# Optimization experiments

Hardware: AMD Instinct MI355X
Metric: run time of the kernel (lower is better)

## Reference

```python
import jax, jax.numpy as jnp
import numpy as np

_LOG2PI = 0.9189385332046727
_NUM_VARS = 256   # D
_NUM_UNITS = 64   # K
_BATCH = 2048     # B
_NUM_LEVELS = 8   # log2(D)


def setup_inputs() -> dict:
    key = jax.random.key(0)
    D, K, B = _NUM_VARS, _NUM_UNITS, _BATCH
    inp = {}
    inp["x"] = jax.random.normal(jax.random.fold_in(key, 0), (B, 1, D), dtype=jnp.float32)
    inp["mu"] = jax.random.normal(jax.random.fold_in(key, 1), (D, K), dtype=jnp.float32)
    inp["log_sigma"] = 0.1 * jax.random.normal(jax.random.fold_in(key, 2), (D, K), dtype=jnp.float32)
    # input-layer bookkeeping: each fold reads one (permuted) variable of x
    inp["in_scope_idx"] = jax.random.permutation(jax.random.fold_in(key, 3), D)[:, None]
    F = D
    for l in range(1, _NUM_LEVELS + 1):
        # fold bookkeeping: irregular pairing of previous-layer folds (permutation -> valid partition)
        inp[f"fold_idx{l}"] = jax.random.permutation(jax.random.fold_in(key, 10 + l), F).reshape(F // 2, 2)
        F //= 2
        inp[f"w{l}"] = jax.random.normal(jax.random.fold_in(key, 100 + l), (F, K, K), dtype=jnp.float32)
    return inp


def _circuit(x, mu, log_sigma, ws, in_scope_idx, fold_idxs):
    # input layer gather: x (B,C,D) -> x[..., idx] (B,C,F,s) -> permute (F,C,B,s)
    xg = jnp.transpose(x[..., in_scope_idx], (2, 1, 0, 3))  # (D,1,B,1)
    xv = xg[:, 0, :, 0]  # (D,B): C=1, scope size 1
    # Gaussian input layer, log densities: (F=D, B, K)
    z = (xv[:, :, None] - mu[:, None, :]) * jnp.exp(-log_sigma)[:, None, :]
    out = -0.5 * z * z - log_sigma[:, None, :] - _LOG2PI
    for fidx, w in zip(fold_idxs, ws):
        # folded Hadamard product layer: gather (F,2,B,K) via bookkeeping, add in log-space
        h = out[fidx].sum(axis=1)  # (F,B,K)
        # folded dense sum layer: y[f,b,j] = logsumexp_k( log softmax(w)[f,j,k] + h[f,b,k] )
        wp = jax.nn.softmax(w, axis=-1)  # (F,K,K)
        m = jnp.max(h, axis=-1, keepdims=True)
        out = jnp.log(jnp.einsum('fbk,fjk->fbj', jnp.exp(h - m), wp)) + m  # (F,B,K)
    # final bookkeeping: (F_out=1, B, K) -> transpose(0,1) -> (B, 1, K)
    return jnp.transpose(out, (1, 0, 2))


def reference(x, mu, log_sigma, w1, w2, w3, w4, w5, w6, w7, w8,
              in_scope_idx, fold_idx1, fold_idx2, fold_idx3, fold_idx4,
              fold_idx5, fold_idx6, fold_idx7, fold_idx8):
    ws = (w1, w2, w3, w4, w5, w6, w7, w8)
    fold_idxs = (fold_idx1, fold_idx2, fold_idx3, fold_idx4,
                 fold_idx5, fold_idx6, fold_idx7, fold_idx8)
    return _circuit(x, mu, log_sigma, ws, in_scope_idx, fold_idxs)
```

## Files before the change

kernel.cpp:

```cpp
#include <hip/hip_runtime.h>
#include <math.h>

#define LOG2PI_F  0.9189385332046727f
#define INV_LN2_F 1.4426950408889634f
#define LN2_F     0.6931471805599453f
#define SROW      72

typedef short bf16x8 __attribute__((ext_vector_type(8)));
typedef float f32x4  __attribute__((ext_vector_type(4)));

struct __align__(16) Op { int w; int c0; int c1; int pad; };

#define WS_WBJ   0u
#define WS_A     2097152u
#define WS_B     2162688u
#define WS_C     2228224u
#define WS_XT    2293760u
#define WS_SCHED 4390912u
#define WS_L4A   4395008u
#define WS_L4M   8589312u

__device__ __forceinline__ short bfr(float f) {
    unsigned int u = __float_as_uint(f);
    u += 0x7fffu + ((u >> 16) & 1u);
    return (short)(u >> 16);
}

__device__ __forceinline__ unsigned pk2(float a, float b) {
    return (unsigned)(unsigned short)bfr(a) | ((unsigned)(unsigned short)bfr(b) << 16);
}

struct F8v { float v[8]; };
__device__ __forceinline__ F8v ld8(const float* p) {
    F8v r;
    float4 a = *(const float4*)p;
    float4 b = *(const float4*)(p + 4);
    r.v[0]=a.x; r.v[1]=a.y; r.v[2]=a.z; r.v[3]=a.w;
    r.v[4]=b.x; r.v[5]=b.y; r.v[6]=b.z; r.v[7]=b.w;
    return r;
}

__device__ __forceinline__ void up8(int4 v, float* o) {
    o[0] = __uint_as_float(((unsigned)v.x) << 16);
    o[1] = __uint_as_float(((unsigned)v.x) & 0xffff0000u);
    o[2] = __uint_as_float(((unsigned)v.y) << 16);
    o[3] = __uint_as_float(((unsigned)v.y) & 0xffff0000u);
    o[4] = __uint_as_float(((unsigned)v.z) << 16);
    o[5] = __uint_as_float(((unsigned)v.z) & 0xffff0000u);
    o[6] = __uint_as_float(((unsigned)v.w) << 16);
    o[7] = __uint_as_float(((unsigned)v.w) & 0xffff0000u);
}

__device__ __forceinline__ float rmax16(const float hv[16]) {
    float m01 = fmaxf(hv[0], hv[1]),  m23 = fmaxf(hv[2], hv[3]);
    float m45 = fmaxf(hv[4], hv[5]),  m67 = fmaxf(hv[6], hv[7]);
    float m89 = fmaxf(hv[8], hv[9]),  mab = fmaxf(hv[10], hv[11]);
    float mcd = fmaxf(hv[12], hv[13]), mef = fmaxf(hv[14], hv[15]);
    float hm = fmaxf(fmaxf(fmaxf(m01, m23), fmaxf(m45, m67)),
                     fmaxf(fmaxf(m89, mab), fmaxf(mcd, mef)));
    hm = fmaxf(hm, __shfl_xor(hm, 16, 64));
    hm = fmaxf(hm, __shfl_xor(hm, 32, 64));
    return hm;
}

__device__ __forceinline__ void pack_p(const float e[16], bf16x8& a0, bf16x8& a1) {
    int4 p0, p1;
    p0.x = __builtin_amdgcn_perm(__float_as_uint(e[1]),  __float_as_uint(e[0]),  0x07060302u);
    p0.y = __builtin_amdgcn_perm(__float_as_uint(e[3]),  __float_as_uint(e[2]),  0x07060302u);
    p0.z = __builtin_amdgcn_perm(__float_as_uint(e[5]),  __float_as_uint(e[4]),  0x07060302u);
    p0.w = __builtin_amdgcn_perm(__float_as_uint(e[7]),  __float_as_uint(e[6]),  0x07060302u);
    p1.x = __builtin_amdgcn_perm(__float_as_uint(e[9]),  __float_as_uint(e[8]),  0x07060302u);
    p1.y = __builtin_amdgcn_perm(__float_as_uint(e[11]), __float_as_uint(e[10]), 0x07060302u);
    p1.z = __builtin_amdgcn_perm(__float_as_uint(e[13]), __float_as_uint(e[12]), 0x07060302u);
    p1.w = __builtin_amdgcn_perm(__float_as_uint(e[15]), __float_as_uint(e[14]), 0x07060302u);
    a0 = *(bf16x8*)&p0;
    a1 = *(bf16x8*)&p1;
}

__global__ __launch_bounds__(256) void prep_kernel(
    const float* __restrict__ w1, const float* __restrict__ w2,
    const float* __restrict__ w3, const float* __restrict__ w4,
    const float* __restrict__ w5, const float* __restrict__ w6,
    const float* __restrict__ w7, const float* __restrict__ w8,
    const float* __restrict__ mu, const float* __restrict__ ls,
    const float* __restrict__ x,  const int* __restrict__ scope,
    const int* __restrict__ f1, const int* __restrict__ f2,
    const int* __restrict__ f3, const int* __restrict__ f4,
    const int* __restrict__ f5, const int* __restrict__ f6,
    const int* __restrict__ f7, const int* __restrict__ f8,
    char* __restrict__ ws)
{
    const int bx = blockIdx.x, t = threadIdx.x;
    if (bx < 255) {
        const int g = bx;
        const float* src;
        if (g < 128)      src = w1 + g * 4096;
        else if (g < 192) src = w2 + (g - 128) * 4096;
        else if (g < 224) src = w3 + (g - 192) * 4096;
        else if (g < 240) src = w4 + (g - 224) * 4096;
        else if (g < 248) src = w5 + (g - 240) * 4096;
        else if (g < 252) src = w6 + (g - 248) * 4096;
        else              src = (g < 254) ? (w7 + (g - 252) * 4096) : w8;

        const int row = t >> 2;
        const int sub = t & 3;
        const float* rp = src + row * 64 + sub * 16;
        float4 v0 = *(const float4*)rp;
        float4 v1 = *(const float4*)(rp + 4);
        float4 v2 = *(const float4*)(rp + 8);
        float4 v3 = *(const float4*)(rp + 12);
        float v[16] = { v0.x, v0.y, v0.z, v0.w,  v1.x, v1.y, v1.z, v1.w,
                        v2.x, v2.y, v2.z, v2.w,  v3.x, v3.y, v3.z, v3.w };
        float mx = fmaxf(fmaxf(fmaxf(fmaxf(v[0], v[1]), fmaxf(v[2], v[3])),
                               fmaxf(fmaxf(v[4], v[5]), fmaxf(v[6], v[7]))),
                         fmaxf(fmaxf(fmaxf(v[8], v[9]), fmaxf(v[10], v[11])),
                               fmaxf(fmaxf(v[12], v[13]), fmaxf(v[14], v[15]))));
        mx = fmaxf(mx, __shfl_xor(mx, 1, 64));
        mx = fmaxf(mx, __shfl_xor(mx, 2, 64));
        float e[16], sm = 0.f;
        #pragma unroll
        for (int i = 0; i < 16; ++i) { e[i] = __expf(v[i] - mx); sm += e[i]; }
        sm += __shfl_xor(sm, 1, 64);
        sm += __shfl_xor(sm, 2, 64);
        const float inv = 1.0f / sm;

        unsigned short* dst = (unsigned short*)(ws + WS_WBJ) + g * 4096;
        #pragma unroll
        for (int c = 0; c < 2; ++c) {
            const int tc = 2 * sub + c;
            const int f  = ((row >> 4) << 1) | (tc >> 2);
            const int ln = ((tc & 3) << 4) | (row & 15);
            int4 pk;
            pk.x = (int)pk2(e[c*8+0] * inv, e[c*8+1] * inv);
            pk.y = (int)pk2(e[c*8+2] * inv, e[c*8+3] * inv);
            pk.z = (int)pk2(e[c*8+4] * inv, e[c*8+5] * inv);
            pk.w = (int)pk2(e[c*8+6] * inv, e[c*8+7] * inv);
            *(int4*)(dst + (size_t)(f * 64 + ln) * 8) = pk;
        }
    } else if (bx < 319) {
        const int idx = (bx - 255) * 256 + t;
        float m = mu[idx], l = ls[idx];
        float is2 = __expf(-2.0f * l);
        ((float*)(ws + WS_A))[idx] = -0.5f * is2 * INV_LN2_F;
        ((float*)(ws + WS_B))[idx] = m * is2 * INV_LN2_F;
        ((float*)(ws + WS_C))[idx] = (-0.5f * m * m * is2 - l - LOG2PI_F) * INV_LN2_F;
    } else if (bx < 575) {
        const int bb = bx - 319;
        const int sd = scope[t];
        float* xT = (float*)(ws + WS_XT);
        #pragma unroll
        for (int i = 0; i < 8; ++i) {
            int b = bb * 8 + i;
            xT[t * 2048 + b] = x[b * 256 + sd];
        }
    } else {
        __shared__ int sf[512];
        for (int i = t; i < 256; i += 256) sf[i]        = f1[i];
        for (int i = t; i < 128; i += 256) sf[256 + i]  = f2[i];
        for (int i = t; i <  64; i += 256) sf[384 + i]  = f3[i];
        for (int i = t; i <  32; i += 256) sf[448 + i]  = f4[i];
        for (int i = t; i <  16; i += 256) sf[480 + i]  = f5[i];
        for (int i = t; i <   8; i += 256) sf[496 + i]  = f6[i];
        for (int i = t; i <   4; i += 256) sf[504 + i]  = f7[i];
        for (int i = t; i <   2; i += 256) sf[508 + i]  = f8[i];
        __syncthreads();
        const int* F1 = &sf[0];   const int* F2 = &sf[256];
        const int* F3 = &sf[384]; const int* F4 = &sf[448];
        const int* F5 = &sf[480]; const int* F6 = &sf[496];
        const int* F7 = &sf[504]; const int* F8 = &sf[508];
        Op* base = (Op*)(ws + WS_SCHED);
        if (t < 16) {
            Op* o = base + t * 15;
            int r0 = F4[2*t], r1 = F4[2*t+1];
            int P[4] = { F3[2*r0], F3[2*r0+1], F3[2*r1], F3[2*r1+1] };
            #pragma unroll
            for (int j = 0; j < 4; ++j) {
                int L0 = F2[2*P[j]], L1 = F2[2*P[j]+1];
                o[2*j]   = { L0 * 4096, F1[2*L0], F1[2*L0+1], 0 };
                o[2*j+1] = { L1 * 4096, F1[2*L1], F1[2*L1+1], 0 };
                o[8+j]   = { (128 + P[j]) * 4096, 0, 0, 0 };
            }
            o[12] = { (192 + r0) * 4096, 0, 0, 0 };
            o[13] = { (192 + r1) * 4096, 0, 0, 0 };
            o[14] = { (224 + t)  * 4096, 0, 0, 0 };
        } else if (t == 16) {
            Op* o = base + 240;
            int g[4] = { F7[2*F8[0]], F7[2*F8[0]+1], F7[2*F8[1]], F7[2*F8[1]+1] };
            #pragma unroll
            for (int a = 0; a < 4; ++a) {
                int l0 = F6[2*g[a]], l1 = F6[2*g[a]+1];
                o[2*a]   = { (240 + l0) * 4096, F5[2*l0], F5[2*l0+1], 0 };
                o[2*a+1] = { (240 + l1) * 4096, F5[2*l1], F5[2*l1+1], 0 };
                o[8+a]   = { (248 + g[a]) * 4096, 0, 0, 0 };
            }
            o[12] = { (252 + F8[0]) * 4096, 0, 0, 0 };
            o[13] = { (252 + F8[1]) * 4096, 0, 0, 0 };
            o[14] = { 254 * 4096, 0, 0, 0 };
        }
    }
}

__device__ __forceinline__ void load_bfrag(const unsigned short* __restrict__ wbJ,
                                           int w, int lane, int4 bf[8]) {
    const int4* wp = (const int4*)(wbJ + w);
    #pragma unroll
    for (int f = 0; f < 8; ++f) bf[f] = wp[f * 64 + lane];
}

__device__ __forceinline__ void prod_norm(const float av[16], const float bv[16],
                                          float MA, float MB,
                                          float p[16], float& Mrow) {
    float pv[16];
    #pragma unroll
    for (int i = 0; i < 16; ++i) pv[i] = av[i] * bv[i];
    const float rm = rmax16(pv);
    const int e = (int)((__float_as_uint(rm) >> 23) & 0xFF) - 127;
    #pragma unroll
    for (int i = 0; i < 16; ++i) p[i] = ldexpf(pv[i], -e);
    Mrow = MA + MB + (float)e;
}

__device__ __forceinline__ void gauss_p(const Op& op,
    const float* __restrict__ xT, const float* __restrict__ Ag,
    const float* __restrict__ Bg, const float* __restrict__ Cg,
    int rowStart, int m, int q, float p[16], float& Mrow)
{
    const int d0 = op.c0, d1 = op.c1;
    const float xv0 = xT[d0 * 2048 + rowStart + m];
    const float xv1 = xT[d1 * 2048 + rowStart + m];
    const float x0s = xv0 * xv0, x1s = xv1 * xv1;
    float hv[16];
    #pragma unroll
    for (int kh = 0; kh < 2; ++kh) {
        const int kb = kh * 32 + q * 8;
        F8v A0 = ld8(Ag + d0*64 + kb), B0 = ld8(Bg + d0*64 + kb);
        F8v C0 = ld8(Cg + d0*64 + kb);
        F8v A1 = ld8(Ag + d1*64 + kb), B1 = ld8(Bg + d1*64 + kb);
        F8v C1 = ld8(Cg + d1*64 + kb);
        #pragma unroll
        for (int i = 0; i < 8; ++i) {
            float t0 = fmaf(A0.v[i], x0s, C0.v[i]);
            t0 = fmaf(B0.v[i], xv0, t0);
            float t1 = fmaf(A1.v[i], x1s, C1.v[i]);
            t1 = fmaf(B1.v[i], xv1, t1);
            hv[kh*8+i] = t0 + t1;
        }
    }
    const float hm = rmax16(hv);
    #pragma unroll
    for (int i = 0; i < 16; ++i) p[i] = __builtin_amdgcn_exp2f(hv[i] - hm);
    Mrow = hm;
}

__device__ __forceinline__ void gprod_p(const Op& op,
    const unsigned short* __restrict__ inAcc, const float* __restrict__ inM,
    int rowStart, int m, int q, float p[16], float& Mrow)
{
    const int4* A4 = (const int4*)(inAcc + (size_t)(op.c0 * 2048 + rowStart + m) * 64);
    const int4* B4 = (const int4*)(inAcc + (size_t)(op.c1 * 2048 + rowStart + m) * 64);
    float av[16], bv[16];
    up8(A4[q], av); up8(A4[4+q], av + 8);
    up8(B4[q], bv); up8(B4[4+q], bv + 8);
    prod_norm(av, bv, inM[op.c0 * 2048 + rowStart + m],
              inM[op.c1 * 2048 + rowStart + m], p, Mrow);
}

__device__ __forceinline__ void slot_prod(const unsigned short* slotS, const float* Mslot,
                                          int sA, int sB, int rowBase, int m, int q,
                                          float p[16], float& Mrow)
{
    const int4* A4 = (const int4*)(slotS + sA * 32 * SROW + (rowBase + m) * SROW);
    const int4* B4 = (const int4*)(slotS + sB * 32 * SROW + (rowBase + m) * SROW);
    float av[16], bv[16];
    up8(A4[q], av); up8(A4[4+q], av + 8);
    up8(B4[q], bv); up8(B4[4+q], bv + 8);
    prod_norm(av, bv, Mslot[sA * 32 + rowBase + m],
              Mslot[sB * 32 + rowBase + m], p, Mrow);
}

__device__ __forceinline__ void mfma8(const float p[16], const int4 bf[8], f32x4 acc[4]) {
    bf16x8 a0, a1;
    pack_p(p, a0, a1);
    #pragma unroll
    for (int jt = 0; jt < 4; ++jt) {
        f32x4 z = {0.f, 0.f, 0.f, 0.f};
        z = __builtin_amdgcn_mfma_f32_16x16x32_bf16(a0, *(bf16x8*)&bf[jt*2+0], z, 0, 0, 0);
        z = __builtin_amdgcn_mfma_f32_16x16x32_bf16(a1, *(bf16x8*)&bf[jt*2+1], z, 0, 0, 0);
        acc[jt] = z;
    }
}

__device__ __forceinline__ void store_slot(unsigned short* slotS, float* Mslot,
                                           int sl, int rowBase, const f32x4 acc[4],
                                           float Mrow, int m, int q)
{
    unsigned short* S = slotS + sl * 32 * SROW;
    #pragma unroll
    for (int jt = 0; jt < 4; ++jt)
        #pragma unroll
        for (int r = 0; r < 4; ++r)
            S[(rowBase + q*4 + r) * SROW + jt*16 + m] = (unsigned short)bfr(acc[jt][r]);
    if (q == 0) Mslot[sl * 32 + rowBase + m] = Mrow;
}

__device__ __forceinline__ void wave_fence() {
    __builtin_amdgcn_wave_barrier();
    __builtin_amdgcn_s_waitcnt(0xC07F);
    __builtin_amdgcn_wave_barrier();
}

template<int MODE>
__global__ __launch_bounds__(256, 4) void circuit_coop(
    const unsigned short* __restrict__ wbJ,
    const Op* __restrict__ schedG, int ntile,
    const float* __restrict__ xT, const float* __restrict__ Ag,
    const float* __restrict__ Bg, const float* __restrict__ Cg,
    const unsigned short* __restrict__ inAcc, const float* __restrict__ inM,
    unsigned short* __restrict__ outAcc, float* __restrict__ outM,
    float* __restrict__ outLog)
{
    __shared__ __align__(16) unsigned short slotS[8 * 32 * SROW];
    __shared__ float Mslot[8 * 32];
    __shared__ Op ops[16];

    const int t    = threadIdx.x;
    const int wv   = t >> 6;
    const int lane = t & 63;
    const int m    = lane & 15;
    const int q    = lane >> 4;
    const int s    = blockIdx.x / ntile;
    const int b0   = (blockIdx.x % ntile) * 32;

    if (t < 15) *(int4*)&ops[t] = ((const int4*)(schedG + s * 15))[t];
    __syncthreads();

    #pragma unroll
    for (int i = 0; i < 2; ++i) {
        const int sl = 2 * wv + i;
        const Op op = ops[sl];
        int4 bf[8];
        load_bfrag(wbJ, op.w, lane, bf);
        float p0[16], p1[16], M0, M1;
        if (MODE == 0) {
            gauss_p(op, xT, Ag, Bg, Cg, b0,      m, q, p0, M0);
            gauss_p(op, xT, Ag, Bg, Cg, b0 + 16, m, q, p1, M1);
        } else {
            gprod_p(op, inAcc, inM, b0,      m, q, p0, M0);
            gprod_p(op, inAcc, inM, b0 + 16, m, q, p1, M1);
        }
        f32x4 acc0[4], acc1[4];
        mfma8(p0, bf, acc0);
        mfma8(p1, bf, acc1);
        store_slot(slotS, Mslot, sl, 0,  acc0, M0, m, q);
        store_slot(slotS, Mslot, sl, 16, acc1, M1, m, q);
    }
    wave_fence();

    {
        const Op op = ops[8 + wv];
        int4 bf[8];
        load_bfrag(wbJ, op.w, lane, bf);
        float p0[16], p1[16], M0, M1;
        slot_prod(slotS, Mslot, 2*wv, 2*wv + 1, 0,  m, q, p0, M0);
        slot_prod(slotS, Mslot, 2*wv, 2*wv + 1, 16, m, q, p1, M1);
        f32x4 acc0[4], acc1[4];
        mfma8(p0, bf, acc0);
        mfma8(p1, bf, acc1);
        store_slot(slotS, Mslot, 2*wv, 0,  acc0, M0, m, q);
        store_slot(slotS, Mslot, 2*wv, 16, acc1, M1, m, q);
    }
    __syncthreads();

    if ((wv & 1) == 0) {
        const int u = wv >> 1;
        const Op op = ops[12 + u];
        int4 bf[8];
        load_bfrag(wbJ, op.w, lane, bf);
        float p0[16], p1[16], M0, M1;
        slot_prod(slotS, Mslot, 4*u, 4*u + 2, 0,  m, q, p0, M0);
        slot_prod(slotS, Mslot, 4*u, 4*u + 2, 16, m, q, p1, M1);
        f32x4 acc0[4], acc1[4];
        mfma8(p0, bf, acc0);
        mfma8(p1, bf, acc1);
        store_slot(slotS, Mslot, 4*u, 0,  acc0, M0, m, q);
        store_slot(slotS, Mslot, 4*u, 16, acc1, M1, m, q);
    }
    __syncthreads();

    if (wv == 0) {
        const Op op = ops[14];
        int4 bf[8];
        load_bfrag(wbJ, op.w, lane, bf);
        float p0[16], p1[16], M0, M1;
        slot_prod(slotS, Mslot, 0, 4, 0,  m, q, p0, M0);
        slot_prod(slotS, Mslot, 0, 4, 16, m, q, p1, M1);
        f32x4 acc0[4], acc1[4];
        mfma8(p0, bf, acc0);
        mfma8(p1, bf, acc1);
        if (MODE == 0) {
            const int rowOff = s * 2048 + b0;
            #pragma unroll
            for (int jt = 0; jt < 4; ++jt)
                #pragma unroll
                for (int r = 0; r < 4; ++r) {
                    outAcc[(size_t)(rowOff +      q*4 + r) * 64 + jt*16 + m] =
                        (unsigned short)bfr(acc0[jt][r]);
                    outAcc[(size_t)(rowOff + 16 + q*4 + r) * 64 + jt*16 + m] =
                        (unsigned short)bfr(acc1[jt][r]);
                }
            if (q == 0) {
                outM[rowOff + m]      = M0;
                outM[rowOff + 16 + m] = M1;
            }
        } else {
            float mr0[4], mr1[4];
            #pragma unroll
            for (int r = 0; r < 4; ++r) {
                mr0[r] = __shfl(M0, q * 4 + r, 64);
                mr1[r] = __shfl(M1, q * 4 + r, 64);
            }
            #pragma unroll
            for (int jt = 0; jt < 4; ++jt)
                #pragma unroll
                for (int r = 0; r < 4; ++r) {
                    outLog[(b0 +      q*4 + r) * 64 + jt*16 + m] =
                        (__builtin_amdgcn_logf(acc0[jt][r]) + mr0[r]) * LN2_F;
                    outLog[(b0 + 16 + q*4 + r) * 64 + jt*16 + m] =
                        (__builtin_amdgcn_logf(acc1[jt][r]) + mr1[r]) * LN2_F;
                }
        }
    }
}

extern "C" void kernel_launch(void* const* d_in, const int* in_sizes, int n_in,
                              void* d_out, int out_size, void* d_ws, size_t ws_size,
                              hipStream_t stream) {
    const float* x     = (const float*)d_in[0];
    const float* mu    = (const float*)d_in[1];
    const float* lsg   = (const float*)d_in[2];
    const int*   scope = (const int*)d_in[3];
    const int*   f1 = (const int*)d_in[4];   const float* w1 = (const float*)d_in[5];
    const int*   f2 = (const int*)d_in[6];   const float* w2 = (const float*)d_in[7];
    const int*   f3 = (const int*)d_in[8];   const float* w3 = (const float*)d_in[9];
    const int*   f4 = (const int*)d_in[10];  const float* w4 = (const float*)d_in[11];
    const int*   f5 = (const int*)d_in[12];  const float* w5 = (const float*)d_in[13];
    const int*   f6 = (const int*)d_in[14];  const float* w6 = (const float*)d_in[15];
    const int*   f7 = (const int*)d_in[16];  const float* w7 = (const float*)d_in[17];
    const int*   f8 = (const int*)d_in[18];  const float* w8 = (const float*)d_in[19];

    char* ws = (char*)d_ws;
    const unsigned short* wbJ = (const unsigned short*)(ws + WS_WBJ);
    const float* Ag  = (const float*)(ws + WS_A);
    const float* Bg  = (const float*)(ws + WS_B);
    const float* Cg  = (const float*)(ws + WS_C);
    const float* xT  = (const float*)(ws + WS_XT);
    const Op*    sch = (const Op*)(ws + WS_SCHED);
    unsigned short* L4A = (unsigned short*)(ws + WS_L4A);
    float*          L4M = (float*)(ws + WS_L4M);

    prep_kernel<<<576, 256, 0, stream>>>(w1, w2, w3, w4, w5, w6, w7, w8,
                                         mu, lsg, x, scope,
                                         f1, f2, f3, f4, f5, f6, f7, f8, ws);

    circuit_coop<0><<<1024, 256, 0, stream>>>(
        wbJ, sch, 64,
        xT, Ag, Bg, Cg,
        nullptr, nullptr,
        L4A, L4M, nullptr);

    circuit_coop<1><<<64, 256, 0, stream>>>(
        wbJ, sch + 240, 64,
        nullptr, nullptr, nullptr, nullptr,
        L4A, L4M,
        nullptr, nullptr, (float*)d_out);
}
```

Baseline: 132.7 us.

## Fuse tail circuit launch into main kernel via last-block-arrival counters

Merges the second circuit kernel launch into the first. Each batch tile keeps an atomic counter, and the last of the 16 subtree blocks for that tile runs the top four levels itself. This removes one kernel launch and the gap between launches, and lets tail work start as soon as a tile's inputs are ready. The cost is atomics, thread fences, and counters that prep_kernel zeroes. Tail work now falls on a few late blocks instead of a separate grid.

Measured after the change: 162.7 us. 22.6% more time.

```diff
diff --git a/kernel.cpp b/kernel.cpp
--- a/kernel.cpp
+++ b/kernel.cpp
@@ -12,6 +12,7 @@
 struct __align__(16) Op { int w; int c0; int c1; int pad; };
 
 #define WS_WBJ   0u
+#define WS_CNT   2088960u
 #define WS_A     2097152u
 #define WS_B     2162688u
 #define WS_C     2228224u
@@ -163,6 +164,7 @@
         for (int i = t; i <   8; i += 256) sf[496 + i]  = f6[i];
         for (int i = t; i <   4; i += 256) sf[504 + i]  = f7[i];
         for (int i = t; i <   2; i += 256) sf[508 + i]  = f8[i];
+        if (t < 64) ((int*)(ws + WS_CNT))[t] = 0;
         __syncthreads();
         const int* F1 = &sf[0];   const int* F2 = &sf[256];
         const int* F3 = &sf[384]; const int* F4 = &sf[448];
@@ -309,19 +311,36 @@
     __builtin_amdgcn_wave_barrier();
 }
 
-template<int MODE>
-__global__ __launch_bounds__(256, 4) void circuit_coop(
+__device__ __forceinline__ void mix2(const Op& op,
     const unsigned short* __restrict__ wbJ,
-    const Op* __restrict__ schedG, int ntile,
+    unsigned short* slotS, float* Mslot,
+    int sA, int sB, int sD, int lane, int m, int q)
+{
+    int4 bf[8];
+    load_bfrag(wbJ, op.w, lane, bf);
+    float p0[16], p1[16], M0, M1;
+    slot_prod(slotS, Mslot, sA, sB, 0,  m, q, p0, M0);
+    slot_prod(slotS, Mslot, sA, sB, 16, m, q, p1, M1);
+    f32x4 acc0[4], acc1[4];
+    mfma8(p0, bf, acc0);
+    mfma8(p1, bf, acc1);
+    store_slot(slotS, Mslot, sD, 0,  acc0, M0, m, q);
+    store_slot(slotS, Mslot, sD, 16, acc1, M1, m, q);
+}
+
+__global__ __launch_bounds__(256, 4) void circuit_fused(
+    const unsigned short* __restrict__ wbJ,
+    const Op* __restrict__ schedG, const Op* __restrict__ tailSched,
+    int ntile,
     const float* __restrict__ xT, const float* __restrict__ Ag,
     const float* __restrict__ Bg, const float* __restrict__ Cg,
-    const unsigned short* __restrict__ inAcc, const float* __restrict__ inM,
-    unsigned short* __restrict__ outAcc, float* __restrict__ outM,
-    float* __restrict__ outLog)
+    unsigned short* __restrict__ L4A, float* __restrict__ L4M,
+    int* __restrict__ counters, float* __restrict__ outLog)
 {
     __shared__ __align__(16) unsigned short slotS[8 * 32 * SROW];
     __shared__ float Mslot[8 * 32];
     __shared__ Op ops[16];
+    __shared__ int arrival;
 
     const int t    = threadIdx.x;
     const int wv   = t >> 6;
@@ -329,7 +348,8 @@
     const int m    = lane & 15;
     const int q    = lane >> 4;
     const int s    = blockIdx.x / ntile;
-    const int b0   = (blockIdx.x % ntile) * 32;
+    const int tile = blockIdx.x % ntile;
+    const int b0   = tile * 32;
 
     if (t < 15) *(int4*)&ops[t] = ((const int4*)(schedG + s * 15))[t];
     __syncthreads();
@@ -341,13 +361,8 @@
         int4 bf[8];
         load_bfrag(wbJ, op.w, lane, bf);
         float p0[16], p1[16], M0, M1;
-        if (MODE == 0) {
-            gauss_p(op, xT, Ag, Bg, Cg, b0,      m, q, p0, M0);
-            gauss_p(op, xT, Ag, Bg, Cg, b0 + 16, m, q, p1, M1);
-        } else {
-            gprod_p(op, inAcc, inM, b0,      m, q, p0, M0);
-            gprod_p(op, inAcc, inM, b0 + 16, m, q, p1, M1);
-        }
+        gauss_p(op, xT, Ag, Bg, Cg, b0,      m, q, p0, M0);
+        gauss_p(op, xT, Ag, Bg, Cg, b0 + 16, m, q, p1, M1);
         f32x4 acc0[4], acc1[4];
         mfma8(p0, bf, acc0);
         mfma8(p1, bf, acc1);
@@ -356,34 +371,12 @@
     }
     wave_fence();
 
-    {
-        const Op op = ops[8 + wv];
-        int4 bf[8];
-        load_bfrag(wbJ, op.w, lane, bf);
-        float p0[16], p1[16], M0, M1;
-        slot_prod(slotS, Mslot, 2*wv, 2*wv + 1, 0,  m, q, p0, M0);
-        slot_prod(slotS, Mslot, 2*wv, 2*wv + 1, 16, m, q, p1, M1);
-        f32x4 acc0[4], acc1[4];
-        mfma8(p0, bf, acc0);
-        mfma8(p1, bf, acc1);
-        store_slot(slotS, Mslot, 2*wv, 0,  acc0, M0, m, q);
-        store_slot(slotS, Mslot, 2*wv, 16, acc1, M1, m, q);
-    }
+    mix2(ops[8 + wv], wbJ, slotS, Mslot, 2*wv, 2*wv + 1, 2*wv, lane, m, q);
     __syncthreads();
 
     if ((wv & 1) == 0) {
         const int u = wv >> 1;
-        const Op op = ops[12 + u];
-        int4 bf[8];
-        load_bfrag(wbJ, op.w, lane, bf);
-        float p0[16], p1[16], M0, M1;
-        slot_prod(slotS, Mslot, 4*u, 4*u + 2, 0,  m, q, p0, M0);
-        slot_prod(slotS, Mslot, 4*u, 4*u + 2, 16, m, q, p1, M1);
-        f32x4 acc0[4], acc1[4];
-        mfma8(p0, bf, acc0);
-        mfma8(p1, bf, acc1);
-        store_slot(slotS, Mslot, 4*u, 0,  acc0, M0, m, q);
-        store_slot(slotS, Mslot, 4*u, 16, acc1, M1, m, q);
+        mix2(ops[12 + u], wbJ, slotS, Mslot, 4*u, 4*u + 2, 4*u, lane, m, q);
     }
     __syncthreads();
 
@@ -397,38 +390,85 @@
         f32x4 acc0[4], acc1[4];
         mfma8(p0, bf, acc0);
         mfma8(p1, bf, acc1);
-        if (MODE == 0) {
-            const int rowOff = s * 2048 + b0;
-            #pragma unroll
-            for (int jt = 0; jt < 4; ++jt)
-                #pragma unroll
-                for (int r = 0; r < 4; ++r) {
-                    outAcc[(size_t)(rowOff +      q*4 + r) * 64 + jt*16 + m] =
-                        (unsigned short)bfr(acc0[jt][r]);
-                    outAcc[(size_t)(rowOff + 16 + q*4 + r) * 64 + jt*16 + m] =
-                        (unsigned short)bfr(acc1[jt][r]);
-                }
-            if (q == 0) {
-                outM[rowOff + m]      = M0;
-                outM[rowOff + 16 + m] = M1;
-            }
-        } else {
-            float mr0[4], mr1[4];
+        const int rowOff = s * 2048 + b0;
+        #pragma unroll
+        for (int jt = 0; jt < 4; ++jt)
             #pragma unroll
             for (int r = 0; r < 4; ++r) {
-                mr0[r] = __shfl(M0, q * 4 + r, 64);
-                mr1[r] = __shfl(M1, q * 4 + r, 64);
+                L4A[(size_t)(rowOff +      q*4 + r) * 64 + jt*16 + m] =
+                    (unsigned short)bfr(acc0[jt][r]);
+                L4A[(size_t)(rowOff + 16 + q*4 + r) * 64 + jt*16 + m] =
+                    (unsigned short)bfr(acc1[jt][r]);
             }
+        if (q == 0) {
+            L4M[rowOff + m]      = M0;
+            L4M[rowOff + 16 + m] = M1;
+        }
+    }
+    __syncthreads();
+
+    if (t == 0) {
+        __threadfence();
+        arrival = atomicAdd(&counters[tile], 1);
+    }
+    __syncthreads();
+    if (arrival != 15) return;
+    __threadfence();
+
+    if (t < 15) *(int4*)&ops[t] = ((const int4*)tailSched)[t];
+    __syncthreads();
+
+    #pragma unroll
+    for (int i = 0; i < 2; ++i) {
+        const int sl = 2 * wv + i;
+        const Op op = ops[sl];
+        int4 bf[8];
+        load_bfrag(wbJ, op.w, lane, bf);
+        float p0[16], p1[16], M0, M1;
+        gprod_p(op, L4A, L4M, b0,      m, q, p0, M0);
+        gprod_p(op, L4A, L4M, b0 + 16, m, q, p1, M1);
+        f32x4 acc0[4], acc1[4];
+        mfma8(p0, bf, acc0);
+        mfma8(p1, bf, acc1);
+        store_slot(slotS, Mslot, sl, 0,  acc0, M0, m, q);
+        store_slot(slotS, Mslot, sl, 16, acc1, M1, m, q);
+    }
+    wave_fence();
+
+    mix2(ops[8 + wv], wbJ, slotS, Mslot, 2*wv, 2*wv + 1, 2*wv, lane, m, q);
+    __syncthreads();
+
+    if ((wv & 1) == 0) {
+        const int u = wv >> 1;
+        mix2(ops[12 + u], wbJ, slotS, Mslot, 4*u, 4*u + 2, 4*u, lane, m, q);
+    }
+    __syncthreads();
+
+    if (wv == 0) {
+        const Op op = ops[14];
+        int4 bf[8];
+        load_bfrag(wbJ, op.w, lane, bf);
+        float p0[16], p1[16], M0, M1;
+        slot_prod(slotS, Mslot, 0, 4, 0,  m, q, p0, M0);
+        slot_prod(slotS, Mslot, 0, 4, 16, m, q, p1, M1);
+        f32x4 acc0[4], acc1[4];
+        mfma8(p0, bf, acc0);
+        mfma8(p1, bf, acc1);
+        float mr0[4], mr1[4];
+        #pragma unroll
+        for (int r = 0; r < 4; ++r) {
+            mr0[r] = __shfl(M0, q * 4 + r, 64);
+            mr1[r] = __shfl(M1, q * 4 + r, 64);
+        }
+        #pragma unroll
+        for (int jt = 0; jt < 4; ++jt)
             #pragma unroll
-            for (int jt = 0; jt < 4; ++jt)
-                #pragma unroll
-                for (int r = 0; r < 4; ++r) {
-                    outLog[(b0 +      q*4 + r) * 64 + jt*16 + m] =
-                        (__builtin_amdgcn_logf(acc0[jt][r]) + mr0[r]) * LN2_F;
-                    outLog[(b0 + 16 + q*4 + r) * 64 + jt*16 + m] =
-                        (__builtin_amdgcn_logf(acc1[jt][r]) + mr1[r]) * LN2_F;
-                }
-        }
+            for (int r = 0; r < 4; ++r) {
+                outLog[(b0 +      q*4 + r) * 64 + jt*16 + m] =
+                    (__builtin_amdgcn_logf(acc0[jt][r]) + mr0[r]) * LN2_F;
+                outLog[(b0 + 16 + q*4 + r) * 64 + jt*16 + m] =
+                    (__builtin_amdgcn_logf(acc1[jt][r]) + mr1[r]) * LN2_F;
+            }
     }
 }
 
@@ -457,20 +497,14 @@
     const Op*    sch = (const Op*)(ws + WS_SCHED);
     unsigned short* L4A = (unsigned short*)(ws + WS_L4A);
     float*          L4M = (float*)(ws + WS_L4M);
+    int*            cnt = (int*)(ws + WS_CNT);
 
     prep_kernel<<<576, 256, 0, stream>>>(w1, w2, w3, w4, w5, w6, w7, w8,
                                          mu, lsg, x, scope,
                                          f1, f2, f3, f4, f5, f6, f7, f8, ws);
 
-    circuit_coop<0><<<1024, 256, 0, stream>>>(
-        wbJ, sch, 64,
+    circuit_fused<<<1024, 256, 0, stream>>>(
+        wbJ, sch, sch + 240, 64,
         xT, Ag, Bg, Cg,
-        nullptr, nullptr,
-        L4A, L4M, nullptr);
-
-    circuit_coop<1><<<64, 256, 0, stream>>>(
-        wbJ, sch + 240, 64,
-        nullptr, nullptr, nullptr, nullptr,
-        L4A, L4M,
-        nullptr, nullptr, (float*)d_out);
-}
+        L4A, L4M, cnt, (float*)d_out);
+}
```
